# Kernel tuning notes

Measured on AMD Instinct MI355X. Metric: run time of the kernel, lower is better.

## Reference

```python
import jax, jax.numpy as jnp
import numpy as np

B, S, D = 2, 2048, 1024
H = 16
HD = D // H
MLP = 4096
EPS_LN = 1e-6
EPS_NORM = 1e-12
LOG_MAX = float(np.log(1.0 / 0.01))  # clamp cap for logit_scale


def setup_inputs() -> dict:
    key = jax.random.key(0)
    ks = jax.random.split(key, 12)
    sd = 0.02
    return {
        "x": jax.random.normal(ks[0], (B, S, D), jnp.float32),
        "wq": jax.random.normal(ks[1], (D, D), jnp.float32) * sd,
        "bq": jnp.zeros((D,), jnp.float32),
        "wk": jax.random.normal(ks[2], (D, D), jnp.float32) * sd,
        "bk": jnp.zeros((D,), jnp.float32),
        "wv": jax.random.normal(ks[3], (D, D), jnp.float32) * sd,
        "bv": jnp.zeros((D,), jnp.float32),
        "wo": jax.random.normal(ks[4], (D, D), jnp.float32) * sd,
        "bo": jnp.zeros((D,), jnp.float32),
        "w1": jax.random.normal(ks[5], (D, MLP), jnp.float32) * sd,
        "b1": jax.random.normal(ks[6], (MLP,), jnp.float32) * 1e-6,
        "w2": jax.random.normal(ks[7], (MLP, D), jnp.float32) * sd,
        "b2": jax.random.normal(ks[8], (D,), jnp.float32) * 1e-6,
        "ln1_g": jnp.ones((D,), jnp.float32),
        "ln1_b": jnp.zeros((D,), jnp.float32),
        "ln2_g": jnp.ones((D,), jnp.float32),
        "ln2_b": jnp.zeros((D,), jnp.float32),
        "logit_scale": jnp.log(10.0 * jnp.ones((H, 1, 1), jnp.float32)),
    }


def _layernorm(x, g, b):
    mu = jnp.mean(x, axis=-1, keepdims=True)
    var = jnp.var(x, axis=-1, keepdims=True)
    return (x - mu) * jax.lax.rsqrt(var + EPS_LN) * g + b


def _l2norm(x):
    n = jnp.linalg.norm(x, axis=-1, keepdims=True)
    return x / jnp.maximum(n, EPS_NORM)


def _split_heads(t):  # [B,S,D] -> [B,H,S,HD]
    return t.reshape(B, S, H, HD).transpose(0, 2, 1, 3)


def reference(x, wq, bq, wk, bk, wv, bv, wo, bo, w1, b1, w2, b2,
              ln1_g, ln1_b, ln2_g, ln2_b, logit_scale):
    h = x
    xn = _layernorm(x, ln1_g, ln1_b)
    q = _split_heads(xn @ wq + bq)
    k = _split_heads(xn @ wk + bk)
    v = _split_heads(xn @ wv + bv)
    # cosine attention: L2-normalize q,k, scale by clamped learnable exp temp
    scores = jnp.einsum("bhqd,bhkd->bhqk", _l2norm(q), _l2norm(k))
    scale = jnp.exp(jnp.minimum(logit_scale, LOG_MAX))  # [H,1,1]
    scores = scores * scale
    probs = jax.nn.softmax(scores, axis=-1)
    ctx = jnp.einsum("bhqk,bhkd->bhqd", probs, v)
    ctx = ctx.transpose(0, 2, 1, 3).reshape(B, S, D)
    x = ctx @ wo + bo + h
    h = x
    xn = _layernorm(x, ln2_g, ln2_b)
    y = jax.nn.gelu(xn @ w1 + b1, approximate=False) @ w2 + b2
    return y + h
```

## Files before the change

### kernel.cpp

```cpp
#include <hip/hip_runtime.h>
#include <hip/hip_bf16.h>
#include <math.h>

typedef unsigned short u16;
typedef unsigned int u32;
typedef __attribute__((ext_vector_type(8))) short bf16x8;
typedef __attribute__((ext_vector_type(4))) float f32x4;
typedef __attribute__((ext_vector_type(16))) float f32x16;

#define S_LEN 2048
#define DM 1024
#define NH 16
#define HD 64
#define MLPD 4096
#define BSZ 2
#define NROWS (BSZ * S_LEN)
#define LOGMAX 4.60517018598809f

__device__ __forceinline__ u16 f2bf(float f) {
  u32 u = __float_as_uint(f);
  u32 r = (u + 0x7fffu + ((u >> 16) & 1u)) >> 16;
  return (u16)r;
}
__device__ __forceinline__ float bf2f(u16 h) { return __uint_as_float(((u32)h) << 16); }
__device__ __forceinline__ u32 pk2(float a, float b) {
  return (u32)f2bf(a) | ((u32)f2bf(b) << 16);
}
__device__ __forceinline__ u32 cvtpk(float a, float b) {
  u32 r;
  asm("v_cvt_pk_bf16_f32 %0, %1, %2" : "=v"(r) : "v"(a), "v"(b));
  return r;
}
__device__ __forceinline__ void gld16(const void* g, void* l) {
  __builtin_amdgcn_global_load_lds(
      (const __attribute__((address_space(1))) void*)g,
      (__attribute__((address_space(3))) void*)l, 16, 0, 0);
}

__global__ __launch_bounds__(256) void ln_bf16(const float* __restrict__ x,
                                               const float* __restrict__ g,
                                               const float* __restrict__ b,
                                               u16* __restrict__ out) {
  const int row = blockIdx.x;
  const int t = threadIdx.x;
  const float* xr = x + (size_t)row * DM;
  float4 v = *reinterpret_cast<const float4*>(xr + t * 4);
  float s = v.x + v.y + v.z + v.w;
  float s2 = v.x * v.x + v.y * v.y + v.z * v.z + v.w * v.w;
#pragma unroll
  for (int off = 32; off > 0; off >>= 1) {
    s += __shfl_down(s, off);
    s2 += __shfl_down(s2, off);
  }
  __shared__ float red[8];
  __shared__ float mv[2];
  const int wid = t >> 6, lane = t & 63;
  if (lane == 0) { red[wid] = s; red[wid + 4] = s2; }
  __syncthreads();
  if (t == 0) {
    float ts = red[0] + red[1] + red[2] + red[3];
    float ts2 = red[4] + red[5] + red[6] + red[7];
    float mu = ts * (1.0f / DM);
    float var = ts2 * (1.0f / DM) - mu * mu;
    mv[0] = mu;
    mv[1] = rsqrtf(var + 1e-6f);
  }
  __syncthreads();
  const float mu = mv[0], rs = mv[1];
  float4 gv = *reinterpret_cast<const float4*>(g + t * 4);
  float4 bv = *reinterpret_cast<const float4*>(b + t * 4);
  float o0 = (v.x - mu) * rs * gv.x + bv.x;
  float o1 = (v.y - mu) * rs * gv.y + bv.y;
  float o2 = (v.z - mu) * rs * gv.z + bv.z;
  float o3 = (v.w - mu) * rs * gv.w + bv.w;
  uint2 o;
  o.x = pk2(o0, o1);
  o.y = pk2(o2, o3);
  *reinterpret_cast<uint2*>(out + (size_t)row * DM + t * 4) = o;
}

__global__ __launch_bounds__(256) void prep_weights(
    const float* __restrict__ wq, const float* __restrict__ wk, const float* __restrict__ wv,
    const float* __restrict__ wo, const float* __restrict__ w1, const float* __restrict__ w2,
    const float* __restrict__ bq, const float* __restrict__ bk, const float* __restrict__ bv,
    u16* __restrict__ wqkv_t, u16* __restrict__ wo_t, u16* __restrict__ w1_t,
    u16* __restrict__ w2_t, float* __restrict__ bqkv) {
  const int tid = threadIdx.x;
  int bid = blockIdx.x;
  if (bid < 12) {
    int i = bid * 256 + tid;
    bqkv[i] = i < 1024 ? bq[i] : (i < 2048 ? bk[i - 1024] : bv[i - 2048]);
  }
  const float* src;
  u16* dst;
  int K, N;
  if (bid < 768) {
    int m = bid >> 8;
    src = (m == 0) ? wq : (m == 1 ? wk : wv);
    dst = wqkv_t + (size_t)m * 1024 * 1024;
    K = 1024; N = 1024;
    bid &= 255;
  } else if (bid < 1024) {
    src = wo; dst = wo_t; K = 1024; N = 1024; bid -= 768;
  } else if (bid < 2048) {
    src = w1; dst = w1_t; K = 1024; N = 4096; bid -= 1024;
  } else {
    src = w2; dst = w2_t; K = 4096; N = 1024; bid -= 2048;
  }
  const int ktiles = K >> 6;
  const int k0 = (bid % ktiles) << 6, n0 = (bid / ktiles) << 6;
  __shared__ float tile[64][65];
#pragma unroll
  for (int p = 0; p < 4; ++p) {
    int r = p * 16 + (tid >> 4), c = (tid & 15) * 4;
    *reinterpret_cast<float4*>(&tile[r][c]) =
        *reinterpret_cast<const float4*>(&src[(size_t)(k0 + r) * N + n0 + c]);
  }
  __syncthreads();
#pragma unroll
  for (int p = 0; p < 4; ++p) {
    int n = p * 16 + (tid >> 4), k = (tid & 15) * 4;
    uint2 o;
    o.x = pk2(tile[k][n], tile[k + 1][n]);
    o.y = pk2(tile[k + 2][n], tile[k + 3][n]);
    *reinterpret_cast<uint2*>(&dst[(size_t)(n0 + n) * K + k0 + k]) = o;
  }
}

#define EPI_BIAS 0
#define EPI_GELU 1
#define EPI_RES 2
#define EPI_QKV 3

template <int EPI, int OUTBF>
__global__ __launch_bounds__(256) void gemm_bf16(
    const u16* __restrict__ A, const u16* __restrict__ Bt,
    const float* __restrict__ bias, const float* __restrict__ res,
    void* __restrict__ Cout, u16* __restrict__ qkx, u16* __restrict__ vtx,
    int M, int N, int K) {
  __shared__ u16 As[2][128 * 32];
  __shared__ u16 Bs[2][128 * 32];
  const int tid = threadIdx.x;
  const int wid = tid >> 6, lane = tid & 63;
  const int n0 = blockIdx.x * 128, m0 = blockIdx.y * 128;
  const int wr = wid >> 1, wc = wid & 1;

  f32x4 acc[4][4];
#pragma unroll
  for (int mi = 0; mi < 4; ++mi)
#pragma unroll
    for (int ni = 0; ni < 4; ++ni)
#pragma unroll
      for (int r = 0; r < 4; ++r) acc[mi][ni][r] = 0.0f;

  const int srow = lane >> 2;
  const int skc = (lane & 3) * 8;
  const int c0 = wid * 2, c1 = wid * 2 + 1;
  const u16* ab0 = A + (size_t)(m0 + c0 * 16 + srow) * K + skc;
  const u16* ab1 = A + (size_t)(m0 + c1 * 16 + srow) * K + skc;
  const u16* bb0 = Bt + (size_t)(n0 + c0 * 16 + srow) * K + skc;
  const u16* bb1 = Bt + (size_t)(n0 + c1 * 16 + srow) * K + skc;

  gld16(ab0, &As[0][c0 * 512]);
  gld16(ab1, &As[0][c1 * 512]);
  gld16(bb0, &Bs[0][c0 * 512]);
  gld16(bb1, &Bs[0][c1 * 512]);
  __syncthreads();

  const int fr = lane & 15, fg = (lane >> 4) * 8;
  int cur = 0;
  for (int k0 = 0; k0 < K; k0 += 32) {
    if (k0 + 32 < K) {
      const int nxt = cur ^ 1;
      gld16(ab0 + k0 + 32, &As[nxt][c0 * 512]);
      gld16(ab1 + k0 + 32, &As[nxt][c1 * 512]);
      gld16(bb0 + k0 + 32, &Bs[nxt][c0 * 512]);
      gld16(bb1 + k0 + 32, &Bs[nxt][c1 * 512]);
    }
    bf16x8 af[4], bfr[4];
#pragma unroll
    for (int mi = 0; mi < 4; ++mi)
      af[mi] = *reinterpret_cast<const bf16x8*>(&As[cur][(wr * 64 + mi * 16 + fr) * 32 + fg]);
#pragma unroll
    for (int ni = 0; ni < 4; ++ni)
      bfr[ni] = *reinterpret_cast<const bf16x8*>(&Bs[cur][(wc * 64 + ni * 16 + fr) * 32 + fg]);
#pragma unroll
    for (int mi = 0; mi < 4; ++mi)
#pragma unroll
      for (int ni = 0; ni < 4; ++ni)
        acc[mi][ni] =
            __builtin_amdgcn_mfma_f32_16x16x32_bf16(af[mi], bfr[ni], acc[mi][ni], 0, 0, 0);
    __syncthreads();
    cur ^= 1;
  }

  const int col0 = n0 + wc * 64 + (lane & 15);
  const int r4 = (lane >> 4) * 4;

  if constexpr (EPI == EPI_QKV) {
    float bias4[4];
#pragma unroll
    for (int ni = 0; ni < 4; ++ni) bias4[ni] = bias[col0 + ni * 16];
    const bool isV = (n0 + wc * 64) >= 2048;
#pragma unroll
    for (int mi = 0; mi < 4; ++mi) {
#pragma unroll
      for (int r = 0; r < 4; ++r) {
        const int row = m0 + wr * 64 + mi * 16 + r4 + r;
        float v[4];
#pragma unroll
        for (int ni = 0; ni < 4; ++ni) v[ni] = acc[mi][ni][r] + bias4[ni];
        if (!isV) {
          float ss = v[0] * v[0] + v[1] * v[1] + v[2] * v[2] + v[3] * v[3];
          ss += __shfl_xor(ss, 1);
          ss += __shfl_xor(ss, 2);
          ss += __shfl_xor(ss, 4);
          ss += __shfl_xor(ss, 8);
          float inv = 1.0f / fmaxf(sqrtf(ss), 1e-12f);
#pragma unroll
          for (int ni = 0; ni < 4; ++ni)
            qkx[(size_t)row * 2048 + col0 + ni * 16] = f2bf(v[ni] * inv);
        } else {
          const int b = row >> 11, sl = row & 2047;
#pragma unroll
          for (int ni = 0; ni < 4; ++ni) {
            const int col = col0 + ni * 16;
            const int h = (col - 2048) >> 6, d = col & 63;
            vtx[((size_t)(b * NH + h) * HD + d) * S_LEN + sl] = f2bf(v[ni]);
          }
        }
      }
    }
    return;
  }

  float bias8[4];
#pragma unroll
  for (int ni = 0; ni < 4; ++ni) bias8[ni] = bias[col0 + ni * 16];
#pragma unroll
  for (int ni = 0; ni < 4; ++ni) {
    const int col = col0 + ni * 16;
    const float bb = bias8[ni];
#pragma unroll
    for (int mi = 0; mi < 4; ++mi) {
      const int row = m0 + wr * 64 + mi * 16 + r4;
#pragma unroll
      for (int r = 0; r < 4; ++r) {
        float v = acc[mi][ni][r] + bb;
        if (EPI == EPI_GELU) v = 0.5f * v * (1.0f + erff(v * 0.70710678118654752f));
        if (EPI == EPI_RES) v += res[(size_t)(row + r) * N + col];
        if (OUTBF)
          ((u16*)Cout)[(size_t)(row + r) * N + col] = f2bf(v);
        else
          ((float*)Cout)[(size_t)(row + r) * N + col] = v;
      }
    }
  }
}

__global__ __launch_bounds__(256) void flash_mfma(const u16* __restrict__ qk,
                                                  const u16* __restrict__ vt,
                                                  const float* __restrict__ lsc,
                                                  u16* __restrict__ ctx) {
  __shared__ u16 Ks[2][64 * 72];
  __shared__ u16 Vt[2][64 * 72];
  __shared__ float den_s[128];
  const int tid = threadIdx.x;
  const int wq = tid >> 6, lane = tid & 63;
  const int lo5 = lane & 31, hi = lane >> 5;
  const int q0 = blockIdx.x * 128;
  const int bh = blockIdx.y, b = bh >> 4, h = bh & 15;
  const float scale = __expf(fminf(lsc[h], LOGMAX));

  bf16x8 qf[4];
#pragma unroll
  for (int dch = 0; dch < 4; ++dch)
    qf[dch] = *reinterpret_cast<const bf16x8*>(
        &qk[(size_t)(b * S_LEN + q0 + wq * 32 + lo5) * 2048 + h * HD + dch * 16 + hi * 8]);

  f32x16 octx[2];
#pragma unroll
  for (int dt = 0; dt < 2; ++dt)
#pragma unroll
    for (int e = 0; e < 16; ++e) octx[dt][e] = 0.0f;
  float den = 0.0f;

  const int sr = tid >> 2, sseg = tid & 3;
  const u16* kbase = qk + (size_t)(b * S_LEN + sr) * 2048 + 1024 + h * HD + sseg * 8;
  const u16* vbase = vt + (size_t)(bh * HD + sr) * S_LEN + sseg * 8;

  {
    uint4 k0 = *reinterpret_cast<const uint4*>(kbase);
    uint4 k1 = *reinterpret_cast<const uint4*>(kbase + 32);
    uint4 v0 = *reinterpret_cast<const uint4*>(vbase);
    uint4 v1 = *reinterpret_cast<const uint4*>(vbase + 32);
    *reinterpret_cast<uint4*>(&Ks[0][sr * 72 + sseg * 8]) = k0;
    *reinterpret_cast<uint4*>(&Ks[0][sr * 72 + 32 + sseg * 8]) = k1;
    *reinterpret_cast<uint4*>(&Vt[0][sr * 72 + sseg * 8]) = v0;
    *reinterpret_cast<uint4*>(&Vt[0][sr * 72 + 32 + sseg * 8]) = v1;
  }
  __syncthreads();

  int buf = 0;
  for (int kt = 0; kt < S_LEN / 64; ++kt) {
    const int nx = (kt + 1) & (S_LEN / 64 - 1);
    uint4 k0 = *reinterpret_cast<const uint4*>(kbase + (size_t)nx * 64 * 2048);
    uint4 k1 = *reinterpret_cast<const uint4*>(kbase + (size_t)nx * 64 * 2048 + 32);
    uint4 v0 = *reinterpret_cast<const uint4*>(vbase + nx * 64);
    uint4 v1 = *reinterpret_cast<const uint4*>(vbase + nx * 64 + 32);

    const u16* Kc = &Ks[buf][0];
    const u16* Vc = &Vt[buf][0];

    f32x16 sc[2];
#pragma unroll
    for (int ktile = 0; ktile < 2; ++ktile)
#pragma unroll
      for (int e = 0; e < 16; ++e) sc[ktile][e] = 0.0f;
#pragma unroll
    for (int ktile = 0; ktile < 2; ++ktile)
#pragma unroll
      for (int dch = 0; dch < 4; ++dch) {
        bf16x8 kf = *reinterpret_cast<const bf16x8*>(
            &Kc[(ktile * 32 + lo5) * 72 + dch * 16 + hi * 8]);
        sc[ktile] = __builtin_amdgcn_mfma_f32_32x32x16_bf16(kf, qf[dch], sc[ktile], 0, 0, 0);
      }

    u32 pk[2][8];
    float ps = 0.0f;
#pragma unroll
    for (int ktile = 0; ktile < 2; ++ktile) {
      float p[16];
#pragma unroll
      for (int r = 0; r < 16; ++r) {
        p[r] = __expf(fmaf(scale, sc[ktile][r], -scale));
        ps += p[r];
      }
#pragma unroll
      for (int n = 0; n < 4; ++n) {
        pk[ktile][n * 2] = cvtpk(p[n * 4], p[n * 4 + 1]);
        pk[ktile][n * 2 + 1] = cvtpk(p[n * 4 + 2], p[n * 4 + 3]);
      }
    }
    ps += __shfl_xor(ps, 32);
    den += ps;

#pragma unroll
    for (int ktile = 0; ktile < 2; ++ktile)
#pragma unroll
      for (int cc = 0; cc < 2; ++cc) {
        u32 o0 = pk[ktile][(2 * cc) * 2], o1 = pk[ktile][(2 * cc) * 2 + 1];
        u32 e0 = pk[ktile][(2 * cc + 1) * 2], e1 = pk[ktile][(2 * cc + 1) * 2 + 1];
        u32 s0 = (u32)__shfl_xor((int)o0, 32);
        u32 s1 = (u32)__shfl_xor((int)o1, 32);
        u32 t0 = (u32)__shfl_xor((int)e0, 32);
        u32 t1 = (u32)__shfl_xor((int)e1, 32);
        union { u32 u[4]; bf16x8 v; } pf;
        pf.u[0] = hi ? t0 : o0;
        pf.u[1] = hi ? t1 : o1;
        pf.u[2] = hi ? e0 : s0;
        pf.u[3] = hi ? e1 : s1;
        const int kvo = (ktile * 2 + cc) * 16 + hi * 8;
#pragma unroll
        for (int dt = 0; dt < 2; ++dt) {
          bf16x8 vf = *reinterpret_cast<const bf16x8*>(&Vc[(dt * 32 + lo5) * 72 + kvo]);
          octx[dt] = __builtin_amdgcn_mfma_f32_32x32x16_bf16(pf.v, vf, octx[dt], 0, 0, 0);
        }
      }

    *reinterpret_cast<uint4*>(&Ks[buf ^ 1][sr * 72 + sseg * 8]) = k0;
    *reinterpret_cast<uint4*>(&Ks[buf ^ 1][sr * 72 + 32 + sseg * 8]) = k1;
    *reinterpret_cast<uint4*>(&Vt[buf ^ 1][sr * 72 + sseg * 8]) = v0;
    *reinterpret_cast<uint4*>(&Vt[buf ^ 1][sr * 72 + 32 + sseg * 8]) = v1;
    __syncthreads();
    buf ^= 1;
  }

  if (hi == 0) den_s[wq * 32 + lo5] = den;
  __syncthreads();
#pragma unroll
  for (int r = 0; r < 16; ++r) {
    const int ql = (r & 3) + 8 * (r >> 2) + 4 * hi;
    const float inv = 1.0f / den_s[wq * 32 + ql];
    const size_t row = (size_t)(b * S_LEN + q0 + wq * 32 + ql);
#pragma unroll
    for (int dt = 0; dt < 2; ++dt)
      ctx[row * DM + h * HD + dt * 32 + lo5] = f2bf(octx[dt][r] * inv);
  }
}

extern "C" void kernel_launch(void* const* d_in, const int* in_sizes, int n_in,
                              void* d_out, int out_size, void* d_ws, size_t ws_size,
                              hipStream_t stream) {
  const float* x    = (const float*)d_in[0];
  const float* wq   = (const float*)d_in[1];
  const float* bq   = (const float*)d_in[2];
  const float* wk   = (const float*)d_in[3];
  const float* bk   = (const float*)d_in[4];
  const float* wv   = (const float*)d_in[5];
  const float* bv   = (const float*)d_in[6];
  const float* wo   = (const float*)d_in[7];
  const float* bo   = (const float*)d_in[8];
  const float* w1   = (const float*)d_in[9];
  const float* b1   = (const float*)d_in[10];
  const float* w2   = (const float*)d_in[11];
  const float* b2   = (const float*)d_in[12];
  const float* ln1g = (const float*)d_in[13];
  const float* ln1b = (const float*)d_in[14];
  const float* ln2g = (const float*)d_in[15];
  const float* ln2b = (const float*)d_in[16];
  const float* lsc  = (const float*)d_in[17];

  char* ws = (char*)d_ws;
  u16* wqkv_t = (u16*)(ws + 0);
  u16* wo_t   = (u16*)(ws + 6291456);
  u16* w1_t   = (u16*)(ws + 8388608);
  u16* w2_t   = (u16*)(ws + 16777216);
  float* bqkv = (float*)(ws + 25165824);
  u16* xn     = (u16*)(ws + 25178112);
  float* x2   = (float*)(ws + 33566720);
  u16* qkbuf  = (u16*)(ws + 50343936);
  u16* vtbuf  = (u16*)(ws + 67121152);
  u16* ctx    = (u16*)(ws + 75509760);
  u16* h1     = qkbuf;

  prep_weights<<<dim3(3072), dim3(256), 0, stream>>>(wq, wk, wv, wo, w1, w2, bq, bk, bv,
                                                     wqkv_t, wo_t, w1_t, w2_t, bqkv);
  ln_bf16<<<dim3(NROWS), dim3(256), 0, stream>>>(x, ln1g, ln1b, xn);
  gemm_bf16<EPI_QKV, 1><<<dim3(3072 / 128, NROWS / 128), dim3(256), 0, stream>>>(
      xn, wqkv_t, bqkv, nullptr, nullptr, qkbuf, vtbuf, NROWS, 3072, 1024);
  flash_mfma<<<dim3(S_LEN / 128, BSZ * NH), dim3(256), 0, stream>>>(qkbuf, vtbuf, lsc, ctx);
  gemm_bf16<EPI_RES, 0><<<dim3(1024 / 128, NROWS / 128), dim3(256), 0, stream>>>(
      ctx, wo_t, bo, x, x2, nullptr, nullptr, NROWS, 1024, 1024);
  ln_bf16<<<dim3(NROWS), dim3(256), 0, stream>>>(x2, ln2g, ln2b, xn);
  gemm_bf16<EPI_GELU, 1><<<dim3(4096 / 128, NROWS / 128), dim3(256), 0, stream>>>(
      xn, w1_t, b1, nullptr, h1, nullptr, nullptr, NROWS, 4096, 1024);
  gemm_bf16<EPI_RES, 0><<<dim3(1024 / 128, NROWS / 128), dim3(256), 0, stream>>>(
      h1, w2_t, b2, x2, (float*)d_out, nullptr, nullptr, NROWS, 1024, 4096);
}
```

Baseline: 422.3 us.

## Split-K the N=1024 GEMMs with a reduce kernel and swizzle workgroups across XCDs

The output-projection and second MLP GEMMs now run with a 2-way K split. Each split writes fp32 partials, and a new elementwise kernel adds the partials, bias and residual. The grid grows from 256 to 512 workgroups, which gives more parallelism and latency hiding on a GPU with many CUs. The cost is extra global-memory traffic for the partials and one more launch per GEMM. All GEMMs and the flash-attention kernel also remap block IDs with a stride-8 swizzle, so neighbouring tiles share the same XCD's L2. The partial buffers reuse workspace regions that are no longer live.

```diff
diff --git a/kernel.cpp b/kernel.cpp
--- a/kernel.cpp
+++ b/kernel.cpp
@@ -131,19 +131,27 @@
 #define EPI_GELU 1
 #define EPI_RES 2
 #define EPI_QKV 3
-
-template <int EPI, int OUTBF>
+#define EPI_PART 4
+
+template <int EPI, int OUTBF, int KSPLIT>
 __global__ __launch_bounds__(256) void gemm_bf16(
     const u16* __restrict__ A, const u16* __restrict__ Bt,
     const float* __restrict__ bias, const float* __restrict__ res,
     void* __restrict__ Cout, u16* __restrict__ qkx, u16* __restrict__ vtx,
+    float* __restrict__ p0, float* __restrict__ p1,
     int M, int N, int K) {
   __shared__ u16 As[2][128 * 32];
   __shared__ u16 Bs[2][128 * 32];
   const int tid = threadIdx.x;
   const int wid = tid >> 6, lane = tid & 63;
-  const int n0 = blockIdx.x * 128, m0 = blockIdx.y * 128;
+  const int nwgxy = gridDim.x * gridDim.y;
+  const int orig = blockIdx.y * gridDim.x + blockIdx.x;
+  const int swz = (orig & 7) * (nwgxy >> 3) + (orig >> 3);
+  const int bx = swz % gridDim.x, by = swz / gridDim.x;
+  const int n0 = bx * 128, m0 = by * 128;
   const int wr = wid >> 1, wc = wid & 1;
+  const int KC = K / KSPLIT;
+  const int klo = (KSPLIT > 1) ? blockIdx.z * KC : 0;
 
   f32x4 acc[4][4];
 #pragma unroll
@@ -156,10 +164,10 @@
   const int srow = lane >> 2;
   const int skc = (lane & 3) * 8;
   const int c0 = wid * 2, c1 = wid * 2 + 1;
-  const u16* ab0 = A + (size_t)(m0 + c0 * 16 + srow) * K + skc;
-  const u16* ab1 = A + (size_t)(m0 + c1 * 16 + srow) * K + skc;
-  const u16* bb0 = Bt + (size_t)(n0 + c0 * 16 + srow) * K + skc;
-  const u16* bb1 = Bt + (size_t)(n0 + c1 * 16 + srow) * K + skc;
+  const u16* ab0 = A + (size_t)(m0 + c0 * 16 + srow) * K + klo + skc;
+  const u16* ab1 = A + (size_t)(m0 + c1 * 16 + srow) * K + klo + skc;
+  const u16* bb0 = Bt + (size_t)(n0 + c0 * 16 + srow) * K + klo + skc;
+  const u16* bb1 = Bt + (size_t)(n0 + c1 * 16 + srow) * K + klo + skc;
 
   gld16(ab0, &As[0][c0 * 512]);
   gld16(ab1, &As[0][c1 * 512]);
@@ -169,8 +177,8 @@
 
   const int fr = lane & 15, fg = (lane >> 4) * 8;
   int cur = 0;
-  for (int k0 = 0; k0 < K; k0 += 32) {
-    if (k0 + 32 < K) {
+  for (int k0 = 0; k0 < KC; k0 += 32) {
+    if (k0 + 32 < KC) {
       const int nxt = cur ^ 1;
       gld16(ab0 + k0 + 32, &As[nxt][c0 * 512]);
       gld16(ab1 + k0 + 32, &As[nxt][c1 * 512]);
@@ -196,6 +204,21 @@
 
   const int col0 = n0 + wc * 64 + (lane & 15);
   const int r4 = (lane >> 4) * 4;
+
+  if constexpr (EPI == EPI_PART) {
+    float* dst = (KSPLIT > 1 && blockIdx.z) ? p1 : p0;
+#pragma unroll
+    for (int ni = 0; ni < 4; ++ni) {
+      const int col = col0 + ni * 16;
+#pragma unroll
+      for (int mi = 0; mi < 4; ++mi) {
+        const int row = m0 + wr * 64 + mi * 16 + r4;
+#pragma unroll
+        for (int r = 0; r < 4; ++r) dst[(size_t)(row + r) * N + col] = acc[mi][ni][r];
+      }
+    }
+    return;
+  }
 
   if constexpr (EPI == EPI_QKV) {
     float bias4[4];
@@ -256,6 +279,20 @@
       }
     }
   }
+}
+
+__global__ __launch_bounds__(256) void reduce_res(
+    const float* __restrict__ p0, const float* __restrict__ p1,
+    const float* __restrict__ bias, const float* __restrict__ res,
+    float* __restrict__ out, int N) {
+  const int i = (blockIdx.x * 256 + threadIdx.x) * 4;
+  float4 a = *reinterpret_cast<const float4*>(p0 + i);
+  float4 b = *reinterpret_cast<const float4*>(p1 + i);
+  float4 r = *reinterpret_cast<const float4*>(res + i);
+  float4 bb = *reinterpret_cast<const float4*>(bias + (i & (N - 1)));
+  float4 o = {a.x + b.x + r.x + bb.x, a.y + b.y + r.y + bb.y,
+              a.z + b.z + r.z + bb.z, a.w + b.w + r.w + bb.w};
+  *reinterpret_cast<float4*>(out + i) = o;
 }
 
 __global__ __launch_bounds__(256) void flash_mfma(const u16* __restrict__ qk,
@@ -268,8 +305,12 @@
   const int tid = threadIdx.x;
   const int wq = tid >> 6, lane = tid & 63;
   const int lo5 = lane & 31, hi = lane >> 5;
-  const int q0 = blockIdx.x * 128;
-  const int bh = blockIdx.y, b = bh >> 4, h = bh & 15;
+  const int nwg = gridDim.x * gridDim.y;
+  const int orig = blockIdx.y * gridDim.x + blockIdx.x;
+  const int swz = (orig & 7) * (nwg >> 3) + (orig >> 3);
+  const int qt = swz % gridDim.x, bh = swz / gridDim.x;
+  const int q0 = qt * 128;
+  const int b = bh >> 4, h = bh & 15;
   const float scale = __expf(fminf(lsc[h], LOGMAX));
 
   bf16x8 qf[4];
@@ -423,18 +464,24 @@
   u16* vtbuf  = (u16*)(ws + 67121152);
   u16* ctx    = (u16*)(ws + 75509760);
   u16* h1     = qkbuf;
+  float* partA = (float*)(ws + 50343936);
+  float* partB = (float*)(ws + 83898368);
+  float* partC = (float*)(ws + 0);
 
   prep_weights<<<dim3(3072), dim3(256), 0, stream>>>(wq, wk, wv, wo, w1, w2, bq, bk, bv,
                                                      wqkv_t, wo_t, w1_t, w2_t, bqkv);
   ln_bf16<<<dim3(NROWS), dim3(256), 0, stream>>>(x, ln1g, ln1b, xn);
-  gemm_bf16<EPI_QKV, 1><<<dim3(3072 / 128, NROWS / 128), dim3(256), 0, stream>>>(
-      xn, wqkv_t, bqkv, nullptr, nullptr, qkbuf, vtbuf, NROWS, 3072, 1024);
+  gemm_bf16<EPI_QKV, 1, 1><<<dim3(3072 / 128, NROWS / 128), dim3(256), 0, stream>>>(
+      xn, wqkv_t, bqkv, nullptr, nullptr, qkbuf, vtbuf, nullptr, nullptr, NROWS, 3072, 1024);
   flash_mfma<<<dim3(S_LEN / 128, BSZ * NH), dim3(256), 0, stream>>>(qkbuf, vtbuf, lsc, ctx);
-  gemm_bf16<EPI_RES, 0><<<dim3(1024 / 128, NROWS / 128), dim3(256), 0, stream>>>(
-      ctx, wo_t, bo, x, x2, nullptr, nullptr, NROWS, 1024, 1024);
+  gemm_bf16<EPI_PART, 0, 2><<<dim3(1024 / 128, NROWS / 128, 2), dim3(256), 0, stream>>>(
+      ctx, wo_t, nullptr, nullptr, nullptr, nullptr, nullptr, partA, partB, NROWS, 1024, 1024);
+  reduce_res<<<dim3(NROWS * 1024 / 1024), dim3(256), 0, stream>>>(partA, partB, bo, x, x2, 1024);
   ln_bf16<<<dim3(NROWS), dim3(256), 0, stream>>>(x2, ln2g, ln2b, xn);
-  gemm_bf16<EPI_GELU, 1><<<dim3(4096 / 128, NROWS / 128), dim3(256), 0, stream>>>(
-      xn, w1_t, b1, nullptr, h1, nullptr, nullptr, NROWS, 4096, 1024);
-  gemm_bf16<EPI_RES, 0><<<dim3(1024 / 128, NROWS / 128), dim3(256), 0, stream>>>(
-      h1, w2_t, b2, x2, (float*)d_out, nullptr, nullptr, NROWS, 1024, 4096);
-}
+  gemm_bf16<EPI_GELU, 1, 1><<<dim3(4096 / 128, NROWS / 128), dim3(256), 0, stream>>>(
+      xn, w1_t, b1, nullptr, h1, nullptr, nullptr, nullptr, nullptr, NROWS, 4096, 1024);
+  gemm_bf16<EPI_PART, 0, 2><<<dim3(1024 / 128, NROWS / 128, 2), dim3(256), 0, stream>>>(
+      h1, w2_t, nullptr, nullptr, nullptr, nullptr, nullptr, partC, partB, NROWS, 1024, 4096);
+  reduce_res<<<dim3(NROWS * 1024 / 1024), dim3(256), 0, stream>>>(partC, partB, b2, x2,
+                                                                  (float*)d_out, 1024);
+}
```

After: 397.2 us. -5.9%, faster.
